# Kernel tuning notes

Hardware: AMD Instinct MI355X
Metric: run time of the kernel (lower is better)

## Reference

```python
import jax, jax.numpy as jnp
import numpy as np

DIM = 768
NUM_HEADS = 12
HEAD_DIM = DIM // NUM_HEADS
SCALE = HEAD_DIM ** -0.5


def setup_inputs() -> dict:
    key = jax.random.key(0)
    k_x, k_qkv, k_proj, k_pb = jax.random.split(key, 4)
    B, N = 4, 2048
    x = jax.random.normal(k_x, (B, N, DIM), dtype=jnp.float32)
    # torch.nn.Linear stores weight as [out_features, in_features]
    w_qkv = jax.random.normal(k_qkv, (3 * DIM, DIM), dtype=jnp.float32) * (DIM ** -0.5)
    w_proj = jax.random.normal(k_proj, (DIM, DIM), dtype=jnp.float32) * (DIM ** -0.5)
    b_proj = jax.random.normal(k_pb, (DIM,), dtype=jnp.float32) * 0.02
    return {"x": x, "w_qkv": w_qkv, "w_proj": w_proj, "b_proj": b_proj}


def reference(x, w_qkv, w_proj, b_proj):
    B, N, C = x.shape
    # qkv projection (no bias): [B, N, 3*C]
    qkv = jnp.einsum('bnc,dc->bnd', x, w_qkv)
    qkv = qkv.reshape(B, N, 3, NUM_HEADS, HEAD_DIM)
    qkv = jnp.transpose(qkv, (2, 0, 3, 1, 4))  # [3, B, H, N, hd]
    q, k, v = qkv[0], qkv[1], qkv[2]
    q = q * SCALE
    attn = jnp.einsum('bhqd,bhkd->bhqk', q, k)          # [B, H, N, N]
    attn = jax.nn.softmax(attn, axis=-1)
    out = jnp.einsum('bhqk,bhkd->bhqd', attn, v)        # [B, H, N, hd]
    out = jnp.transpose(out, (0, 2, 1, 3)).reshape(B, N, C)
    return jnp.einsum('bnc,dc->bnd', out, w_proj) + b_proj
```

## Files before the change

### kernel.cpp

```cpp
#include <hip/hip_runtime.h>

typedef unsigned short u16;
typedef __attribute__((ext_vector_type(8))) short short8;
typedef __attribute__((ext_vector_type(4))) float f32x4;
typedef __attribute__((ext_vector_type(8))) float f32x8;
typedef __attribute__((ext_vector_type(2))) unsigned int u32x2;

#define MFMA(a, b, c) __builtin_amdgcn_mfma_f32_16x16x32_bf16((a), (b), (c), 0, 0, 0)

__device__ __forceinline__ u16 f2bf(float f) {
    union { float f; unsigned int u; } v; v.f = f;
    unsigned int u = v.u;
    return (u16)((u + 0x7fffu + ((u >> 16) & 1u)) >> 16);
}

__device__ __forceinline__ float exp2fast(float x) {
#if __has_builtin(__builtin_amdgcn_exp2f)
    return __builtin_amdgcn_exp2f(x);
#else
    return exp2f(x);
#endif
}

__device__ __forceinline__ unsigned int cvtpk(float lo, float hi) {
    unsigned int r;
    asm("v_cvt_pk_bf16_f32 %0, %1, %2" : "=v"(r) : "v"(lo), "v"(hi));
    return r;
}

__device__ __forceinline__ void gload16(const void* g, void* l) {
    __builtin_amdgcn_global_load_lds((const __attribute__((address_space(1))) unsigned int*)g,
                                     (__attribute__((address_space(3))) unsigned int*)l,
                                     16, 0, 0);
}

#define N1 6291456
#define N2 1769472
#define N3 589824

__global__ __launch_bounds__(256) void cvt_bf16(const float* __restrict__ x,
                                                const float* __restrict__ wq,
                                                const float* __restrict__ wp,
                                                u16* __restrict__ xb,
                                                u16* __restrict__ wqb,
                                                u16* __restrict__ wpb) {
    size_t i = ((size_t)blockIdx.x * 256 + threadIdx.x) * 8;
    const float* src;
    u16* dst;
    size_t off;
    if (i < N1)            { src = x;  dst = xb;  off = i; }
    else if (i < N1 + N2)  { src = wq; dst = wqb; off = i - N1; }
    else                   { src = wp; dst = wpb; off = i - N1 - N2; }
    f32x8 v = *(const f32x8*)(src + off);
    short8 o;
#pragma unroll
    for (int j = 0; j < 8; ++j) o[j] = (short)f2bf(v[j]);
    *(short8*)(dst + off) = o;
}

__global__ __launch_bounds__(256) void qkv_gemm(const u16* __restrict__ X,
                                                const u16* __restrict__ W,
                                                u16* __restrict__ Qb,
                                                u16* __restrict__ Kb,
                                                u16* __restrict__ Vt) {
    __shared__ __align__(16) u16 abuf[128 * 64];
    __shared__ __align__(16) u16 bbuf[128 * 64];

    const int id = blockIdx.x;
    const int swz = (id & 7) * 144 + (id >> 3);
    const int m0 = (swz & 63) * 128;
    const int n0 = (swz >> 6) * 128;
    const int tid = threadIdx.x;
    const int lane = tid & 63;
    const int w = tid >> 6;
    const int wm = (w >> 1) * 64, wn = (w & 1) * 64;
    const int lrow = lane & 15, rgrp = lane >> 4;

    const int sr = lane >> 3;
    const int schunk = (lane & 7) ^ (sr & 7);
    const u16* asrc = X + (size_t)(m0 + w * 32 + sr) * 768 + schunk * 8;
    const u16* bsrc = W + (size_t)(n0 + w * 32 + sr) * 768 + schunk * 8;
    u16* adst = abuf + (w * 32) * 64;
    u16* bdst = bbuf + (w * 32) * 64;

    f32x4 acc[4][4] = {};

    for (int k0 = 0; k0 < 768; k0 += 64) {
        __syncthreads();
#pragma unroll
        for (int p = 0; p < 4; ++p) {
            gload16(asrc + (size_t)(p * 8) * 768 + k0, adst + (p * 8) * 64);
            gload16(bsrc + (size_t)(p * 8) * 768 + k0, bdst + (p * 8) * 64);
        }
        __syncthreads();

        __builtin_amdgcn_s_setprio(1);
#pragma unroll
        for (int ks = 0; ks < 2; ++ks) {
            short8 a[4], b[4];
            const int cs = (ks * 4 + rgrp);
#pragma unroll
            for (int mf = 0; mf < 4; ++mf)
                a[mf] = *(const short8*)(abuf + (wm + mf * 16 + lrow) * 64 + ((cs ^ (lrow & 7)) * 8));
#pragma unroll
            for (int nf = 0; nf < 4; ++nf)
                b[nf] = *(const short8*)(bbuf + (wn + nf * 16 + lrow) * 64 + ((cs ^ (lrow & 7)) * 8));
#pragma unroll
            for (int mf = 0; mf < 4; ++mf)
#pragma unroll
                for (int nf = 0; nf < 4; ++nf)
                    acc[mf][nf] = MFMA(a[mf], b[nf], acc[mf][nf]);
        }
        __builtin_amdgcn_s_setprio(0);
    }

    const int which = n0 / 768;
    if (which < 2) {
        u16* dst = (which == 0) ? Qb : Kb;
        const float scl = (which == 0) ? 0.180336879f : 1.0f;
#pragma unroll
        for (int mf = 0; mf < 4; ++mf)
#pragma unroll
            for (int nf = 0; nf < 4; ++nf)
#pragma unroll
                for (int r = 0; r < 4; ++r) {
                    int m = m0 + wm + mf * 16 + rgrp * 4 + r;
                    int d = n0 + wn + nf * 16 + lrow - which * 768;
                    int h = d >> 6, e = d & 63;
                    int bb = m >> 11, nseq = m & 2047;
                    dst[(((size_t)bb * 12 + h) * 2048 + nseq) * 64 + e] = f2bf(acc[mf][nf][r] * scl);
                }
    } else {
#pragma unroll
        for (int mf = 0; mf < 4; ++mf)
#pragma unroll
            for (int nf = 0; nf < 4; ++nf)
#pragma unroll
                for (int r = 0; r < 4; ++r) {
                    int m = m0 + wm + mf * 16 + rgrp * 4 + r;
                    int d = n0 + wn + nf * 16 + lrow - 1536;
                    int h = d >> 6, e = d & 63;
                    int bb = m >> 11, nseq = m & 2047;
                    Vt[(((size_t)bb * 12 + h) * 64 + e) * 2048 + nseq] = f2bf(acc[mf][nf][r]);
                }
    }
}

__global__ __launch_bounds__(512) void attn_kernel(const u16* __restrict__ Qb,
                                                   const u16* __restrict__ Kb,
                                                   const u16* __restrict__ Vt,
                                                   u16* __restrict__ AO) {
    __shared__ __align__(16) u16 kbuf[2][4096];
    __shared__ __align__(16) u16 vbuf[2][4096];
    __shared__ __align__(16) u16 pbuf[8][16 * 72];

    const int id = blockIdx.x;
    const int xcd = id & 7, per = id >> 3;
    const int bh = xcd * 6 + (per >> 4);
    const int q0 = (per & 15) * 128;
    const int tid = threadIdx.x;
    const int lane = tid & 63;
    const int w = tid >> 6;
    const int lrow = lane & 15, rgrp = lane >> 4, lk = rgrp * 8;

    const u16* Qp = Qb + (size_t)bh * 2048 * 64;
    const u16* Kp = Kb + (size_t)bh * 2048 * 64;
    const u16* Vp = Vt + (size_t)bh * 64 * 2048;

    const int srow = w * 8 + (lane >> 3);
    const int schunk = lane & 7;
    const int sswz = schunk ^ (srow & 7);
    const u16* ksrc = Kp + srow * 64 + sswz * 8;
    const u16* vsrc = Vp + (size_t)srow * 2048 + sswz * 8;
    const int woff = w * 512;

    const int row0 = q0 + w * 16;
    short8 qf[2];
#pragma unroll
    for (int ks = 0; ks < 2; ++ks)
        qf[ks] = *(const short8*)(Qp + (size_t)(row0 + lrow) * 64 + ks * 32 + lk);

    f32x4 oacc[4] = {};
    float lrun = 0.f;

    u16* Pw = pbuf[w];
    const int swz = lane & 7;

    gload16(ksrc, kbuf[0] + woff);
    gload16(vsrc, vbuf[0] + woff);

    for (int kt = 0; kt < 32; ++kt) {
        const int cur = kt & 1;
        __syncthreads();
        if (kt + 1 < 32) {
            gload16(ksrc + (kt + 1) * 4096, kbuf[cur ^ 1] + woff);
            gload16(vsrc + (kt + 1) * 64,   vbuf[cur ^ 1] + woff);
        }

        const u16* kb = kbuf[cur];
        f32x4 sacc[4];
#pragma unroll
        for (int nf = 0; nf < 4; ++nf) sacc[nf] = f32x4{-16.f, -16.f, -16.f, -16.f};
        __builtin_amdgcn_s_setprio(1);
#pragma unroll
        for (int nf = 0; nf < 4; ++nf)
#pragma unroll
            for (int ks = 0; ks < 2; ++ks) {
                short8 kf = *(const short8*)(kb + (nf * 16 + lrow) * 64 + ((ks * 4 + rgrp) ^ swz) * 8);
                sacc[nf] = MFMA(kf, qf[ks], sacc[nf]);
            }
        __builtin_amdgcn_s_setprio(0);

#pragma unroll
        for (int nf = 0; nf < 4; ++nf) {
            float p0 = exp2fast(sacc[nf][0]);
            float p1 = exp2fast(sacc[nf][1]);
            float p2 = exp2fast(sacc[nf][2]);
            float p3 = exp2fast(sacc[nf][3]);
            lrun += (p0 + p1) + (p2 + p3);
            u32x2 pk;
            pk.x = cvtpk(p0, p1);
            pk.y = cvtpk(p2, p3);
            *(u32x2*)&Pw[lrow * 72 + nf * 16 + rgrp * 4] = pk;
        }

        const u16* vb = vbuf[cur];
        __builtin_amdgcn_s_setprio(1);
#pragma unroll
        for (int ks = 0; ks < 2; ++ks) {
            short8 pa = *(const short8*)&Pw[lrow * 72 + ks * 32 + lk];
#pragma unroll
            for (int df = 0; df < 4; ++df) {
                short8 vf = *(const short8*)(vb + (df * 16 + lrow) * 64 + ((ks * 4 + rgrp) ^ swz) * 8);
                oacc[df] = MFMA(pa, vf, oacc[df]);
            }
        }
        __builtin_amdgcn_s_setprio(0);
    }

    float l = lrun;
    l += __shfl_xor(l, 16);
    l += __shfl_xor(l, 32);
    float linv[4];
#pragma unroll
    for (int r = 0; r < 4; ++r) linv[r] = 1.f / __shfl(l, rgrp * 4 + r);

    const int b = bh / 12, h = bh % 12;
#pragma unroll
    for (int r = 0; r < 4; ++r) {
        int row = row0 + rgrp * 4 + r;
#pragma unroll
        for (int df = 0; df < 4; ++df)
            AO[((size_t)b * 2048 + row) * 768 + h * 64 + df * 16 + lrow] = f2bf(oacc[df][r] * linv[r]);
    }
}

__global__ __launch_bounds__(256) void proj_gemm(const u16* __restrict__ A,
                                                 const u16* __restrict__ W,
                                                 const float* __restrict__ bias,
                                                 float* __restrict__ out) {
    __shared__ __align__(16) u16 abuf[128 * 64];
    __shared__ __align__(16) u16 bbuf[128 * 64];

    const int id = blockIdx.x;
    const int swz = (id & 7) * 48 + (id >> 3);
    const int m0 = (swz & 63) * 128;
    const int n0 = (swz >> 6) * 128;
    const int tid = threadIdx.x;
    const int lane = tid & 63;
    const int w = tid >> 6;
    const int wm = (w >> 1) * 64, wn = (w & 1) * 64;
    const int lrow = lane & 15, rgrp = lane >> 4;

    const int sr = lane >> 3;
    const int schunk = (lane & 7) ^ (sr & 7);
    const u16* asrc = A + (size_t)(m0 + w * 32 + sr) * 768 + schunk * 8;
    const u16* bsrc = W + (size_t)(n0 + w * 32 + sr) * 768 + schunk * 8;
    u16* adst = abuf + (w * 32) * 64;
    u16* bdst = bbuf + (w * 32) * 64;

    f32x4 acc[4][4] = {};

    for (int k0 = 0; k0 < 768; k0 += 64) {
        __syncthreads();
#pragma unroll
        for (int p = 0; p < 4; ++p) {
            gload16(asrc + (size_t)(p * 8) * 768 + k0, adst + (p * 8) * 64);
            gload16(bsrc + (size_t)(p * 8) * 768 + k0, bdst + (p * 8) * 64);
        }
        __syncthreads();

        __builtin_amdgcn_s_setprio(1);
#pragma unroll
        for (int ks = 0; ks < 2; ++ks) {
            short8 a[4], b[4];
            const int cs = (ks * 4 + rgrp);
#pragma unroll
            for (int mf = 0; mf < 4; ++mf)
                a[mf] = *(const short8*)(abuf + (wm + mf * 16 + lrow) * 64 + ((cs ^ (lrow & 7)) * 8));
#pragma unroll
            for (int nf = 0; nf < 4; ++nf)
                b[nf] = *(const short8*)(bbuf + (wn + nf * 16 + lrow) * 64 + ((cs ^ (lrow & 7)) * 8));
#pragma unroll
            for (int mf = 0; mf < 4; ++mf)
#pragma unroll
                for (int nf = 0; nf < 4; ++nf)
                    acc[mf][nf] = MFMA(a[mf], b[nf], acc[mf][nf]);
        }
        __builtin_amdgcn_s_setprio(0);
    }

#pragma unroll
    for (int nf = 0; nf < 4; ++nf) {
        int d = n0 + wn + nf * 16 + lrow;
        float bv = bias[d];
#pragma unroll
        for (int mf = 0; mf < 4; ++mf)
#pragma unroll
            for (int r = 0; r < 4; ++r) {
                int m = m0 + wm + mf * 16 + rgrp * 4 + r;
                out[(size_t)m * 768 + d] = acc[mf][nf][r] + bv;
            }
    }
}

extern "C" void kernel_launch(void* const* d_in, const int* in_sizes, int n_in,
                              void* d_out, int out_size, void* d_ws, size_t ws_size,
                              hipStream_t stream) {
    const float* x      = (const float*)d_in[0];
    const float* w_qkv  = (const float*)d_in[1];
    const float* w_proj = (const float*)d_in[2];
    const float* b_proj = (const float*)d_in[3];
    float* out = (float*)d_out;

    const size_t per = (size_t)48 * 2048 * 64;
    u16* Qb  = (u16*)d_ws;
    u16* Kb  = Qb + per;
    u16* Vt  = Kb + per;
    u16* XB  = Vt + per;
    u16* AO  = XB;
    u16* WQB = XB + per;
    u16* WPB = WQB + (size_t)N2;

    cvt_bf16<<<4224, 256, 0, stream>>>(x, w_qkv, w_proj, XB, WQB, WPB);
    qkv_gemm<<<1152, 256, 0, stream>>>(XB, WQB, Qb, Kb, Vt);
    attn_kernel<<<768, 512, 0, stream>>>(Qb, Kb, Vt, AO);
    proj_gemm<<<384, 256, 0, stream>>>(AO, WPB, b_proj, out);
}
```

Baseline: 150.7 us.

## Switch attention to 32x32 MFMA with register-resident P and retile proj GEMM

The attention kernel now uses 32x32x16 bf16 MFMA with 4 waves of 32 query rows each. The probability tile stays in registers, and v_permlane32_swap rearranges it into the A-operand layout, removing the LDS round trip through pbuf. K/V staging doubles per thread to fit the 256-thread block. Separately, proj_gemm moves to 64x128 tiles with twice as many blocks, aiming for better CU occupancy on the small GEMM. The risks are higher register pressure from f32x16 accumulators and fewer waves per block to hide latency.

```diff
diff --git a/kernel.cpp b/kernel.cpp
--- a/kernel.cpp
+++ b/kernel.cpp
@@ -1,12 +1,14 @@
 #include <hip/hip_runtime.h>
 
 typedef unsigned short u16;
+typedef unsigned int u32;
 typedef __attribute__((ext_vector_type(8))) short short8;
 typedef __attribute__((ext_vector_type(4))) float f32x4;
 typedef __attribute__((ext_vector_type(8))) float f32x8;
-typedef __attribute__((ext_vector_type(2))) unsigned int u32x2;
+typedef __attribute__((ext_vector_type(16))) float f32x16;
 
 #define MFMA(a, b, c) __builtin_amdgcn_mfma_f32_16x16x32_bf16((a), (b), (c), 0, 0, 0)
+#define MFMA32(a, b, c) __builtin_amdgcn_mfma_f32_32x32x16_bf16((a), (b), (c), 0, 0, 0)
 
 __device__ __forceinline__ u16 f2bf(float f) {
     union { float f; unsigned int u; } v; v.f = f;
@@ -22,8 +24,8 @@
 #endif
 }
 
-__device__ __forceinline__ unsigned int cvtpk(float lo, float hi) {
-    unsigned int r;
+__device__ __forceinline__ u32 cvtpk(float lo, float hi) {
+    u32 r;
     asm("v_cvt_pk_bf16_f32 %0, %1, %2" : "=v"(r) : "v"(lo), "v"(hi));
     return r;
 }
@@ -146,13 +148,12 @@
     }
 }
 
-__global__ __launch_bounds__(512) void attn_kernel(const u16* __restrict__ Qb,
+__global__ __launch_bounds__(256) void attn_kernel(const u16* __restrict__ Qb,
                                                    const u16* __restrict__ Kb,
                                                    const u16* __restrict__ Vt,
                                                    u16* __restrict__ AO) {
     __shared__ __align__(16) u16 kbuf[2][4096];
     __shared__ __align__(16) u16 vbuf[2][4096];
-    __shared__ __align__(16) u16 pbuf[8][16 * 72];
 
     const int id = blockIdx.x;
     const int xcd = id & 7, per = id >> 3;
@@ -161,97 +162,99 @@
     const int tid = threadIdx.x;
     const int lane = tid & 63;
     const int w = tid >> 6;
-    const int lrow = lane & 15, rgrp = lane >> 4, lk = rgrp * 8;
+    const int l31 = lane & 31, h = lane >> 5;
 
     const u16* Qp = Qb + (size_t)bh * 2048 * 64;
     const u16* Kp = Kb + (size_t)bh * 2048 * 64;
     const u16* Vp = Vt + (size_t)bh * 64 * 2048;
 
     const int srow = w * 8 + (lane >> 3);
-    const int schunk = lane & 7;
-    const int sswz = schunk ^ (srow & 7);
+    const int sswz = (lane & 7) ^ (srow & 7);
     const u16* ksrc = Kp + srow * 64 + sswz * 8;
     const u16* vsrc = Vp + (size_t)srow * 2048 + sswz * 8;
     const int woff = w * 512;
 
-    const int row0 = q0 + w * 16;
-    short8 qf[2];
-#pragma unroll
-    for (int ks = 0; ks < 2; ++ks)
-        qf[ks] = *(const short8*)(Qp + (size_t)(row0 + lrow) * 64 + ks * 32 + lk);
-
-    f32x4 oacc[4] = {};
+    const int row0 = q0 + w * 32;
+    short8 qf[4];
+#pragma unroll
+    for (int s = 0; s < 4; ++s)
+        qf[s] = *(const short8*)(Qp + (size_t)(row0 + l31) * 64 + s * 16 + h * 8);
+
+    f32x16 oacc[2] = {};
     float lrun = 0.f;
-
-    u16* Pw = pbuf[w];
-    const int swz = lane & 7;
+    const int rswz = l31 & 7;
 
     gload16(ksrc, kbuf[0] + woff);
+    gload16(ksrc + 2048, kbuf[0] + woff + 2048);
     gload16(vsrc, vbuf[0] + woff);
+    gload16(vsrc + 32 * 2048, vbuf[0] + woff + 2048);
 
     for (int kt = 0; kt < 32; ++kt) {
         const int cur = kt & 1;
         __syncthreads();
         if (kt + 1 < 32) {
-            gload16(ksrc + (kt + 1) * 4096, kbuf[cur ^ 1] + woff);
-            gload16(vsrc + (kt + 1) * 64,   vbuf[cur ^ 1] + woff);
+            gload16(ksrc + (kt + 1) * 4096,        kbuf[cur ^ 1] + woff);
+            gload16(ksrc + (kt + 1) * 4096 + 2048, kbuf[cur ^ 1] + woff + 2048);
+            gload16(vsrc + (kt + 1) * 64,             vbuf[cur ^ 1] + woff);
+            gload16(vsrc + (kt + 1) * 64 + 32 * 2048, vbuf[cur ^ 1] + woff + 2048);
         }
 
         const u16* kb = kbuf[cur];
-        f32x4 sacc[4];
-#pragma unroll
-        for (int nf = 0; nf < 4; ++nf) sacc[nf] = f32x4{-16.f, -16.f, -16.f, -16.f};
+        f32x16 st[2] = {};
         __builtin_amdgcn_s_setprio(1);
 #pragma unroll
-        for (int nf = 0; nf < 4; ++nf)
-#pragma unroll
-            for (int ks = 0; ks < 2; ++ks) {
-                short8 kf = *(const short8*)(kb + (nf * 16 + lrow) * 64 + ((ks * 4 + rgrp) ^ swz) * 8);
-                sacc[nf] = MFMA(kf, qf[ks], sacc[nf]);
+        for (int t = 0; t < 2; ++t)
+#pragma unroll
+            for (int s = 0; s < 4; ++s) {
+                short8 kf = *(const short8*)(kb + (t * 32 + l31) * 64 + (((s * 2 + h) ^ rswz) * 8));
+                st[t] = MFMA32(kf, qf[s], st[t]);
             }
         __builtin_amdgcn_s_setprio(0);
 
 #pragma unroll
-        for (int nf = 0; nf < 4; ++nf) {
-            float p0 = exp2fast(sacc[nf][0]);
-            float p1 = exp2fast(sacc[nf][1]);
-            float p2 = exp2fast(sacc[nf][2]);
-            float p3 = exp2fast(sacc[nf][3]);
-            lrun += (p0 + p1) + (p2 + p3);
-            u32x2 pk;
-            pk.x = cvtpk(p0, p1);
-            pk.y = cvtpk(p2, p3);
-            *(u32x2*)&Pw[lrow * 72 + nf * 16 + rgrp * 4] = pk;
+        for (int t = 0; t < 2; ++t) {
+            float rs = 0.f;
+#pragma unroll
+            for (int r = 0; r < 16; ++r) {
+                float p = exp2fast(st[t][r]);
+                st[t][r] = p;
+                rs += p;
+            }
+            lrun += rs;
         }
 
         const u16* vb = vbuf[cur];
         __builtin_amdgcn_s_setprio(1);
 #pragma unroll
-        for (int ks = 0; ks < 2; ++ks) {
-            short8 pa = *(const short8*)&Pw[lrow * 72 + ks * 32 + lk];
-#pragma unroll
-            for (int df = 0; df < 4; ++df) {
-                short8 vf = *(const short8*)(vb + (df * 16 + lrow) * 64 + ((ks * 4 + rgrp) ^ swz) * 8);
-                oacc[df] = MFMA(pa, vf, oacc[df]);
+        for (int s = 0; s < 4; ++s) {
+            const int t = s >> 1, rb = (s & 1) * 8;
+            u32 a  = cvtpk(st[t][rb + 0], st[t][rb + 1]);
+            u32 a2 = cvtpk(st[t][rb + 2], st[t][rb + 3]);
+            u32 b  = cvtpk(st[t][rb + 4], st[t][rb + 5]);
+            u32 b2 = cvtpk(st[t][rb + 6], st[t][rb + 7]);
+            asm volatile("v_permlane32_swap_b32 %0, %1" : "+v"(a), "+v"(b));
+            asm volatile("v_permlane32_swap_b32 %0, %1" : "+v"(a2), "+v"(b2));
+            union { u32 u[4]; short8 s8; } pf;
+            pf.u[0] = a; pf.u[1] = a2; pf.u[2] = b; pf.u[3] = b2;
+#pragma unroll
+            for (int dt = 0; dt < 2; ++dt) {
+                short8 vf = *(const short8*)(vb + (dt * 32 + l31) * 64 + (((s * 2 + h) ^ rswz) * 8));
+                oacc[dt] = MFMA32(pf.s8, vf, oacc[dt]);
             }
         }
         __builtin_amdgcn_s_setprio(0);
     }
 
     float l = lrun;
-    l += __shfl_xor(l, 16);
     l += __shfl_xor(l, 32);
-    float linv[4];
-#pragma unroll
-    for (int r = 0; r < 4; ++r) linv[r] = 1.f / __shfl(l, rgrp * 4 + r);
-
-    const int b = bh / 12, h = bh % 12;
-#pragma unroll
-    for (int r = 0; r < 4; ++r) {
-        int row = row0 + rgrp * 4 + r;
-#pragma unroll
-        for (int df = 0; df < 4; ++df)
-            AO[((size_t)b * 2048 + row) * 768 + h * 64 + df * 16 + lrow] = f2bf(oacc[df][r] * linv[r]);
+    const int b = bh / 12, hh = bh % 12;
+#pragma unroll
+    for (int r = 0; r < 16; ++r) {
+        const int q = (r & 3) + 8 * (r >> 2) + 4 * h;
+        const float inv = 1.f / __shfl(l, q);
+        const size_t base = ((size_t)b * 2048 + row0 + q) * 768 + hh * 64 + l31;
+        AO[base]      = f2bf(oacc[0][r] * inv);
+        AO[base + 32] = f2bf(oacc[1][r] * inv);
     }
 }
 
@@ -259,66 +262,69 @@
                                                  const u16* __restrict__ W,
                                                  const float* __restrict__ bias,
                                                  float* __restrict__ out) {
-    __shared__ __align__(16) u16 abuf[128 * 64];
+    __shared__ __align__(16) u16 abuf[64 * 64];
     __shared__ __align__(16) u16 bbuf[128 * 64];
 
     const int id = blockIdx.x;
-    const int swz = (id & 7) * 48 + (id >> 3);
-    const int m0 = (swz & 63) * 128;
-    const int n0 = (swz >> 6) * 128;
+    const int swz = (id & 7) * 96 + (id >> 3);
+    const int m0 = (swz & 127) * 64;
+    const int n0 = (swz >> 7) * 128;
     const int tid = threadIdx.x;
     const int lane = tid & 63;
     const int w = tid >> 6;
-    const int wm = (w >> 1) * 64, wn = (w & 1) * 64;
     const int lrow = lane & 15, rgrp = lane >> 4;
 
-    const int sr = lane >> 3;
-    const int schunk = (lane & 7) ^ (sr & 7);
-    const u16* asrc = A + (size_t)(m0 + w * 32 + sr) * 768 + schunk * 8;
-    const u16* bsrc = W + (size_t)(n0 + w * 32 + sr) * 768 + schunk * 8;
-    u16* adst = abuf + (w * 32) * 64;
-    u16* bdst = bbuf + (w * 32) * 64;
-
-    f32x4 acc[4][4] = {};
+    const int sra = w * 16 + (lane >> 3);
+    const int srb = w * 32 + (lane >> 3);
+    const int aswz = (lane & 7) ^ (sra & 7);
+    const int bswz = (lane & 7) ^ (srb & 7);
+    const u16* asrc = A + (size_t)(m0 + sra) * 768 + aswz * 8;
+    const u16* bsrc = W + (size_t)(n0 + srb) * 768 + bswz * 8;
+    u16* adst = abuf + sra * 64 - (size_t)(lane >> 3) * 64 + ((lane >> 3) * 64);
+    u16* adst0 = abuf + (w * 16) * 64;
+    u16* bdst0 = bbuf + (w * 32) * 64;
+
+    f32x4 acc[4][2] = {};
 
     for (int k0 = 0; k0 < 768; k0 += 64) {
         __syncthreads();
 #pragma unroll
-        for (int p = 0; p < 4; ++p) {
-            gload16(asrc + (size_t)(p * 8) * 768 + k0, adst + (p * 8) * 64);
-            gload16(bsrc + (size_t)(p * 8) * 768 + k0, bdst + (p * 8) * 64);
-        }
+        for (int p = 0; p < 2; ++p)
+            gload16(asrc + (size_t)(p * 8) * 768 + k0, adst0 + (p * 8) * 64);
+#pragma unroll
+        for (int p = 0; p < 4; ++p)
+            gload16(bsrc + (size_t)(p * 8) * 768 + k0, bdst0 + (p * 8) * 64);
         __syncthreads();
 
         __builtin_amdgcn_s_setprio(1);
 #pragma unroll
         for (int ks = 0; ks < 2; ++ks) {
-            short8 a[4], b[4];
+            short8 a[4], b[2];
             const int cs = (ks * 4 + rgrp);
 #pragma unroll
             for (int mf = 0; mf < 4; ++mf)
-                a[mf] = *(const short8*)(abuf + (wm + mf * 16 + lrow) * 64 + ((cs ^ (lrow & 7)) * 8));
-#pragma unroll
-            for (int nf = 0; nf < 4; ++nf)
-                b[nf] = *(const short8*)(bbuf + (wn + nf * 16 + lrow) * 64 + ((cs ^ (lrow & 7)) * 8));
+                a[mf] = *(const short8*)(abuf + (mf * 16 + lrow) * 64 + ((cs ^ (lrow & 7)) * 8));
+#pragma unroll
+            for (int nf = 0; nf < 2; ++nf)
+                b[nf] = *(const short8*)(bbuf + (w * 32 + nf * 16 + lrow) * 64 + ((cs ^ (lrow & 7)) * 8));
 #pragma unroll
             for (int mf = 0; mf < 4; ++mf)
 #pragma unroll
-                for (int nf = 0; nf < 4; ++nf)
+                for (int nf = 0; nf < 2; ++nf)
                     acc[mf][nf] = MFMA(a[mf], b[nf], acc[mf][nf]);
         }
         __builtin_amdgcn_s_setprio(0);
     }
 
 #pragma unroll
-    for (int nf = 0; nf < 4; ++nf) {
-        int d = n0 + wn + nf * 16 + lrow;
-        float bv = bias[d];
+    for (int nf = 0; nf < 2; ++nf) {
+        const int d = n0 + w * 32 + nf * 16 + lrow;
+        const float bv = bias[d];
 #pragma unroll
         for (int mf = 0; mf < 4; ++mf)
 #pragma unroll
             for (int r = 0; r < 4; ++r) {
-                int m = m0 + wm + mf * 16 + rgrp * 4 + r;
+                const int m = m0 + mf * 16 + rgrp * 4 + r;
                 out[(size_t)m * 768 + d] = acc[mf][nf][r] + bv;
             }
     }
@@ -344,6 +350,6 @@
 
     cvt_bf16<<<4224, 256, 0, stream>>>(x, w_qkv, w_proj, XB, WQB, WPB);
     qkv_gemm<<<1152, 256, 0, stream>>>(XB, WQB, Qb, Kb, Vt);
-    attn_kernel<<<768, 512, 0, stream>>>(Qb, Kb, Vt, AO);
-    proj_gemm<<<384, 256, 0, stream>>>(AO, WPB, b_proj, out);
-}
+    attn_kernel<<<768, 256, 0, stream>>>(Qb, Kb, Vt, AO);
+    proj_gemm<<<768, 256, 0, stream>>>(AO, WPB, b_proj, out);
+}
```

Measured after the change: 153.8 us. +2.0%, slower.
